# Optimization experiments

Hardware: AMD Instinct MI355X
Metric: run time of the kernel (lower is better)

Reference implementation:

```python
import jax, jax.numpy as jnp
import numpy as np

B, E, N, H, F = 16, 8192, 384, 32, 16


def _forward(edge_feat, node_feat, edge_index, edge_mask, num_ligand_atoms,
             structural_w, plip_protein_w, plip_ligand_w, plip_inter_w,
             loc_w, virtual_w, W1, b1, W2, b2):
    n_graph, max_e, _ = edge_feat.shape
    n_node = node_feat.shape[1]
    codes = edge_feat[:, :, :3].astype(jnp.int32)          # [B,E,3] edge type codes
    dist = edge_feat[:, :, 3:4]                            # [B,E,1]
    c0, c1, c2 = codes[..., 0], codes[..., 1], codes[..., 2]
    src = edge_index[:, 0, :]                              # [B,E]
    tgt = edge_index[:, 1, :]
    nl = num_ligand_atoms[:, None]
    src_lig = src < nl
    tgt_lig = tgt < nl

    # structural edges: c0 in {0,1} -> idx = c0*4 + c1*2 + c2
    struct_idx = jnp.clip(c0 * 4 + c1 * 2 + c2, 0, 19)
    struct_emb = structural_w[struct_idx]                  # [B,E,H]

    # PLIP edges: c0 == 5 -> table chosen by ligand membership + location emb
    pi = jnp.clip(c1, 0, 14)
    both_lig = src_lig & tgt_lig
    both_prot = (~src_lig) & (~tgt_lig)
    plip_emb = jnp.where(both_lig[..., None], plip_ligand_w[pi],
                         jnp.where(both_prot[..., None], plip_protein_w[pi], plip_inter_w[pi]))
    loc = jnp.where(both_lig, 0, jnp.where(both_prot, 1, 2))
    plip_emb = plip_emb + loc_w[loc]

    is_struct = (c0 == 0) | (c0 == 1)
    is_plip = c0 == 5
    type_emb = jnp.where(is_struct[..., None], struct_emb,
                         jnp.where(is_plip[..., None], plip_emb, 0.0))

    # distance MLP: Linear(1,H) -> ReLU -> Linear(H,H)
    h = jax.nn.relu(dist @ W1.T + b1)                      # [B,E,H]
    dist_emb = h @ W2.T + b2

    keep = edge_mask & ~((src == 0) & (tgt == 0))
    edge_emb = jnp.where(keep[..., None], type_emb + dist_emb, 0.0)  # [B,E,H]

    # scatter-add into bias [B, N+1, N+1, H] (symmetric), offset +1 for graph token
    s1 = src + 1
    t1 = tgt + 1
    valid = edge_mask & (src >= 0) & (src < n_node) & (tgt >= 0) & (tgt < n_node)
    s_idx = jnp.where(valid, s1, 0)
    t_idx = jnp.where(valid, t1, 0)
    val = jnp.where(valid[..., None], edge_emb, 0.0)
    b_idx = jnp.broadcast_to(jnp.arange(n_graph)[:, None], (n_graph, max_e))

    bias = jnp.zeros((n_graph, n_node + 1, n_node + 1, H), dtype=edge_feat.dtype)
    bias = bias.at[b_idx, s_idx, t_idx].add(val)
    bias = bias.at[b_idx, t_idx, s_idx].add(val)

    # graph-token virtual distance
    t = virtual_w[0]                                       # [H]
    bias = bias.at[:, 1:, 0, :].add(t)
    bias = bias.at[:, 0, :, :].add(t)
    return jnp.transpose(bias, (0, 3, 1, 2))               # [B,H,N+1,N+1]


def setup_inputs() -> dict:
    key = jax.random.key(0)
    ks = jax.random.split(key, 16)
    c0 = jax.random.randint(ks[0], (B, E), 0, 7)
    c1 = jnp.where(c0 <= 1, jax.random.randint(ks[1], (B, E), 0, 2),
                   jax.random.randint(ks[2], (B, E), 0, 15))
    c2 = jax.random.randint(ks[3], (B, E), 0, 2)
    dist = jax.random.uniform(ks[4], (B, E, 1)) * 10.0
    edge_feat = jnp.concatenate([jnp.stack([c0, c1, c2], -1).astype(jnp.float32), dist], -1)
    edge_index = jax.random.randint(ks[5], (B, 2, E), 0, N).astype(jnp.int32)
    edge_mask = jax.random.uniform(ks[6], (B, E)) > 0.1
    num_ligand_atoms = jax.random.randint(ks[7], (B,), 1, N).astype(jnp.int32)
    node_feat = jax.random.normal(ks[8], (B, N, F), dtype=jnp.float32)
    std_e = 0.02
    std_l = 0.02 / np.sqrt(12.0)
    structural_w = (jax.random.normal(ks[9], (20, H)) * std_e).at[0].set(0.0)
    plip_protein_w = (jax.random.normal(ks[10], (15, H)) * std_e).at[0].set(0.0)
    plip_ligand_w = (jax.random.normal(ks[11], (15, H)) * std_e).at[0].set(0.0)
    plip_inter_w = (jax.random.normal(ks[12], (15, H)) * std_e).at[0].set(0.0)
    loc_w = jax.random.normal(ks[13], (4, H)) * std_e
    virtual_w = jax.random.normal(ks[14], (1, H)) * std_e
    W1 = jax.random.normal(ks[15], (H, 1)) * std_l
    W2 = jax.random.normal(jax.random.fold_in(key, 99), (H, H)) * std_l
    b1 = jnp.zeros((H,), jnp.float32)
    b2 = jnp.zeros((H,), jnp.float32)
    return dict(edge_feat=edge_feat, node_feat=node_feat, edge_index=edge_index,
                edge_mask=edge_mask, num_ligand_atoms=num_ligand_atoms,
                structural_w=structural_w, plip_protein_w=plip_protein_w,
                plip_ligand_w=plip_ligand_w, plip_inter_w=plip_inter_w,
                loc_w=loc_w, virtual_w=virtual_w, W1=W1, b1=b1, W2=W2, b2=b2)


def reference(edge_feat, node_feat, edge_index, edge_mask, num_ligand_atoms,
              structural_w, plip_protein_w, plip_ligand_w, plip_inter_w,
              loc_w, virtual_w, W1, b1, W2, b2):
    return _forward(edge_feat, node_feat, edge_index, edge_mask, num_ligand_atoms,
                    structural_w, plip_protein_w, plip_ligand_w, plip_inter_w,
                    loc_w, virtual_w, W1, b1, W2, b2)
```

## Files before the change

### kernel.cpp

```cpp
#include <hip/hip_runtime.h>
#include <hip/hip_bf16.h>

#define B_  16
#define E_  8192
#define NN_ 384
#define N1_ 385
#define H_  32
#define HH_ 16
#define PLANE_ (N1_ * N1_)
#define TOTAL_ (B_ * H_ * PLANE_)
#define CAP_ 128
#define NBIN_ (B_ * N1_)
#define STRIDE_ 396
#define TS_ 21
#define CHUNK_ 5
#define NCH_ 77

#define WS_COUNTS 0
#define WS_T      32768
#define WS_A      33024
#define WS_B      (33024 + 33*32*4)
#define WS_BINS2  65536
#define WS_NEED   ((size_t)WS_BINS2 + (size_t)NBIN_*CAP_*8)


__global__ __launch_bounds__(256) void prep_kernel(
    const float* __restrict__ W1, const float* __restrict__ b1,
    const float* __restrict__ W2, const float* __restrict__ b2,
    float* __restrict__ T, float* __restrict__ A, float* __restrict__ Bv,
    int* __restrict__ counts)
{
    int g = blockIdx.x * 256 + threadIdx.x;
    if (g < NBIN_) counts[g] = 0;

    if (blockIdx.x == 0) {
        __shared__ float sTv[32], sT[32], sW1[32], sb1[32];
        int tid = threadIdx.x;
        if (tid < 32) {
            float w = W1[tid], b = b1[tid];
            sW1[tid] = w; sb1[tid] = b;
            sTv[tid] = (w != 0.0f) ? (-b / w) : -3.402823e38f;
        }
        __syncthreads();
        if (tid < 32) {
            float t = sTv[tid];
            int rank = 0;
            for (int j = 0; j < 32; ++j) {
                float tj = sTv[j];
                rank += (tj < t || (tj == t && j < tid)) ? 1 : 0;
            }
            sT[rank] = t;
        }
        __syncthreads();
        if (tid < 32) T[tid] = sT[tid];
        for (int idx = tid; idx < 33 * 32; idx += 256) {
            int s = idx >> 5, h = idx & 31;
            float m;
            if (s == 0)       m = sT[0] - 1.0f;
            else if (s == 32) m = sT[31] + 1.0f;
            else              m = 0.5f * (sT[s - 1] + sT[s]);
            float alpha = b2[h], beta = 0.0f;
            for (int k = 0; k < 32; ++k) {
                float w = sW1[k], b = sb1[k];
                bool act = (w > 0.0f) ? (m > -b / w)
                         : (w < 0.0f) ? (m < -b / w) : (b > 0.0f);
                if (act) {
                    float w2 = W2[h * 32 + k];
                    alpha = fmaf(w2, b, alpha);
                    beta  = fmaf(w2, w, beta);
                }
            }
            A[idx] = alpha; Bv[idx] = beta;
        }
    }
}

__global__ __launch_bounds__(256) void bin_kernel(
    const float4* __restrict__ edge_feat,
    const int*    __restrict__ edge_index,
    const void*   __restrict__ edge_mask,
    const int*    __restrict__ nlig,
    const float*  __restrict__ T,
    int* __restrict__ counts, int2* __restrict__ bins2)
{
    int lane = threadIdx.x & 63;
    int probe = ((const int*)edge_mask)[lane];
    bool byte_mask = __any(probe != 0 && probe != 1);

    int gid = blockIdx.x * blockDim.x + threadIdx.x;
    int b = gid >> 13, e = gid & (E_ - 1);
    bool m = byte_mask ? (((const unsigned char*)edge_mask)[gid] != 0)
                       : (((const int*)edge_mask)[gid] != 0);
    if (!m) return;
    int src = edge_index[(b * 2 + 0) * E_ + e];
    int tgt = edge_index[(b * 2 + 1) * E_ + e];
    if (src < 0 || src >= NN_ || tgt < 0 || tgt >= NN_) return;
    if (src == 0 && tgt == 0) return;

    float4 ef = edge_feat[gid];
    int c0 = (int)ef.x, c1 = (int)ef.y, c2 = (int)ef.z;
    float dist = ef.w;

    int r;
    if (c0 == 0 || c0 == 1) {
        r = min(max(c0 * 4 + c1 * 2 + c2, 0), 19);
    } else if (c0 == 5) {
        int pi = min(max(c1, 0), 14);
        int nl = nlig[b];
        bool sl = src < nl, tl = tgt < nl;
        int loc = (sl && tl) ? 0 : ((!sl && !tl) ? 1 : 2);
        r = 20 + loc * 15 + pi;
    } else r = 65;

    int lo = 0;
#pragma unroll
    for (int q = 0; q < 8; ++q) {
        float4 tv = *reinterpret_cast<const float4*>(T + 4 * q);
        lo += (tv.x < dist) ? 1 : 0;
        lo += (tv.y < dist) ? 1 : 0;
        lo += (tv.z < dist) ? 1 : 0;
        lo += (tv.w < dist) ? 1 : 0;
    }

    int s1 = src + 1, t1 = tgt + 1;
    int db = __float_as_int(dist);
    int base = (lo << 16) | (r << 9);
    int bin1 = b * N1_ + s1, bin2i = b * N1_ + t1;
    int p = atomicAdd(&counts[bin1], 1);
    if (p < CAP_) bins2[bin1 * CAP_ + p] = make_int2(base | t1, db);
    p = atomicAdd(&counts[bin2i], 1);
    if (p < CAP_) bins2[bin2i * CAP_ + p] = make_int2(base | s1, db);
}

__global__ __launch_bounds__(512, 8) void chunk_kernel(
    const float* __restrict__ structural_w,
    const float* __restrict__ plip_protein_w,
    const float* __restrict__ plip_ligand_w,
    const float* __restrict__ plip_inter_w,
    const float* __restrict__ loc_w,
    const float* __restrict__ virtual_w,
    const float* __restrict__ A,
    const float* __restrict__ Bv,
    const int*   __restrict__ counts,
    const int2*  __restrict__ bins2,
    float* __restrict__ out)
{
    __shared__ float4 srow4[HH_ * (STRIDE_ / 4)];
    __shared__ float sA[33 * TS_], sB[33 * TS_];
    __shared__ float sType[66 * TS_];
    float* srow = reinterpret_cast<float*>(srow4);

    int bid = blockIdx.x;
    int chunk = bid % NCH_;
    int rest  = bid / NCH_;
    int half = rest & 1;
    int b = rest >> 1;
    int h0 = half << 4;
    int tid = threadIdx.x;
    int wv = tid >> 6, lane = tid & 63;

    int i0 = chunk * CHUNK_;
    int rowid0 = b * N1_ + i0;

    int cnts[CHUNK_];
#pragma unroll
    for (int ii = 0; ii < CHUNK_; ++ii) cnts[ii] = counts[rowid0 + ii];

    for (int idx = tid; idx < 33 * 16; idx += 512) {
        int s = idx >> 4, hh = idx & 15;
        sA[s * TS_ + hh] = A[s * 32 + h0 + hh];
        sB[s * TS_ + hh] = Bv[s * 32 + h0 + hh];
    }
    for (int idx = tid; idx < 66 * 16; idx += 512) {
        int r = idx >> 4, hh = idx & 15;
        float v;
        if (r < 20) v = structural_w[r * 32 + h0 + hh];
        else if (r < 65) {
            int t2 = r - 20;
            int loc = t2 / 15, pi = t2 - loc * 15;
            const float* pw = (loc == 0) ? plip_ligand_w
                            : (loc == 1) ? plip_protein_w : plip_inter_w;
            v = pw[pi * 32 + h0 + hh] + loc_w[loc * 32 + h0 + hh];
        } else v = 0.0f;
        sType[r * TS_ + hh] = v;
    }

    int hh_q = lane & 1;
    int slot = lane >> 1;
    int hhg  = (wv << 1) | hh_q;
    int hq   = h0 + hhg;
    float* sW = srow + (wv << 1) * STRIDE_;

    int rw = lane >> 5;
    int sl = lane & 31;
    int hw = h0 + (wv << 1) + rw;
    float vw0 = virtual_w[h0 + (wv << 1)];
    float vw1 = virtual_w[h0 + (wv << 1) + 1];

    __syncthreads();

#pragma unroll 1
    for (int ii = 0; ii < CHUNK_; ++ii) {
        int i = i0 + ii;
        int rowid = rowid0 + ii;

#pragma unroll
        for (int r = 0; r < 2; ++r) {
            float vwr = (r == 0) ? vw0 : vw1;
            float fill = (i == 0) ? vwr : 0.0f;
            float4 f4 = make_float4(fill, fill, fill, fill);
            float4* rp = reinterpret_cast<float4*>(sW + r * STRIDE_);
            for (int c = lane; c < STRIDE_ / 4; c += 64) rp[c] = f4;
        }
        if (i != 0 && lane < 2) {
            int hr = h0 + (wv << 1) + lane;
            int off = (4 - ((hr + i) & 3)) & 3;
            sW[lane * STRIDE_ + 4 - off] = (lane == 0) ? vw0 : vw1;
        }

        int cnt = cnts[ii]; cnt = cnt < CAP_ ? cnt : CAP_;
        int offq = (4 - ((hq + i) & 3)) & 3;
        int base = hh_q * STRIDE_ + 4 - offq;
        for (int j = slot; j < cnt; j += 32) {
            int2 e2 = bins2[rowid * CAP_ + j];
            float dist = __int_as_float(e2.y);
            int other = e2.x & 0x1FF;
            int r     = (e2.x >> 9) & 0x7F;
            int lo    = e2.x >> 16;
            float acc = fmaf(dist, sB[lo * TS_ + hhg], sA[lo * TS_ + hhg])
                      + sType[r * TS_ + hhg];
            atomicAdd(&sW[base + other], acc);
        }

        {
            const float* rr = sW + rw * STRIDE_;
            float* dst = out + ((size_t)(b * H_ + hw)) * PLANE_ + (size_t)i * N1_;
            int off = (4 - ((hw + i) & 3)) & 3;
            if (sl < off) dst[sl] = rr[4 - off + sl];
            int nvec = (N1_ - off) >> 2;
            for (int q = sl; q < nvec; q += 32) {
                float4 v = *reinterpret_cast<const float4*>(rr + 4 + 4 * q);
                *reinterpret_cast<float4*>(dst + off + 4 * q) = v;
            }
            int done = off + (nvec << 2);
            int rem = N1_ - done;
            if (sl < rem) dst[done + sl] = rr[4 + 4 * nvec + sl];
        }
    }
}


__global__ __launch_bounds__(256) void init_out_kernel(
    float* __restrict__ out, const float* __restrict__ virtual_w)
{
    unsigned int tid = blockIdx.x * blockDim.x + threadIdx.x;
    unsigned int base = tid * 4u;
    if (base >= (unsigned int)TOTAL_) return;
    float4 v; float* pv = &v.x;
#pragma unroll
    for (int u = 0; u < 4; ++u) {
        unsigned int idx = base + u;
        unsigned int bh     = idx / (unsigned int)PLANE_;
        unsigned int within = idx - bh * (unsigned int)PLANE_;
        unsigned int h = bh & (H_ - 1);
        unsigned int i = within / (unsigned int)N1_;
        unsigned int j = within - i * (unsigned int)N1_;
        pv[u] = (i == 0u || j == 0u) ? virtual_w[h] : 0.0f;
    }
    *reinterpret_cast<float4*>(out + base) = v;
}

__global__ __launch_bounds__(256) void edge_kernel(
    const float4* __restrict__ edge_feat, const int* __restrict__ edge_index,
    const void* __restrict__ edge_mask, const int* __restrict__ nlig,
    const float* __restrict__ structural_w, const float* __restrict__ plip_protein_w,
    const float* __restrict__ plip_ligand_w, const float* __restrict__ plip_inter_w,
    const float* __restrict__ loc_w, const float* __restrict__ W1,
    const float* __restrict__ b1, const float* __restrict__ W2,
    const float* __restrict__ b2, float* __restrict__ out)
{
    __shared__ float sW2[H_ * H_];
    __shared__ float sW1[H_], sb1[H_], sb2[H_];
    __shared__ float sStruct[20 * H_];
    __shared__ float sPlipP[15 * H_], sPlipL[15 * H_], sPlipI[15 * H_];
    __shared__ float sLoc[4 * H_];

    for (int i = threadIdx.x; i < H_ * H_; i += blockDim.x) sW2[i] = W2[i];
    if (threadIdx.x < H_) {
        sW1[threadIdx.x] = W1[threadIdx.x];
        sb1[threadIdx.x] = b1[threadIdx.x];
        sb2[threadIdx.x] = b2[threadIdx.x];
    }
    for (int i = threadIdx.x; i < 20 * H_; i += blockDim.x) sStruct[i] = structural_w[i];
    for (int i = threadIdx.x; i < 15 * H_; i += blockDim.x) {
        sPlipP[i] = plip_protein_w[i]; sPlipL[i] = plip_ligand_w[i]; sPlipI[i] = plip_inter_w[i];
    }
    for (int i = threadIdx.x; i < 4 * H_; i += blockDim.x) sLoc[i] = loc_w[i];

    int lane = threadIdx.x & 63;
    int probe = ((const int*)edge_mask)[lane];
    bool byte_mask = __any(probe != 0 && probe != 1);
    __syncthreads();

    int gid = blockIdx.x * blockDim.x + threadIdx.x;
    int b = gid >> 13, e = gid & (E_ - 1);
    bool m = byte_mask ? (((const unsigned char*)edge_mask)[gid] != 0)
                       : (((const int*)edge_mask)[gid] != 0);
    if (!m) return;
    int src = edge_index[(b * 2 + 0) * E_ + e];
    int tgt = edge_index[(b * 2 + 1) * E_ + e];
    if (src < 0 || src >= NN_ || tgt < 0 || tgt >= NN_) return;
    if (src == 0 && tgt == 0) return;

    float4 ef = edge_feat[gid];
    int c0 = (int)ef.x, c1 = (int)ef.y, c2 = (int)ef.z;
    float dist = ef.w;
    const float* type_ptr = nullptr; const float* loc_ptr = nullptr;
    if (c0 == 0 || c0 == 1) {
        int si = min(max(c0 * 4 + c1 * 2 + c2, 0), 19);
        type_ptr = &sStruct[si * H_];
    } else if (c0 == 5) {
        int pi = min(max(c1, 0), 14);
        int nl = nlig[b];
        bool sl = src < nl, tl = tgt < nl;
        const float* pw; int loc;
        if (sl && tl)        { pw = sPlipL; loc = 0; }
        else if (!sl && !tl) { pw = sPlipP; loc = 1; }
        else                 { pw = sPlipI; loc = 2; }
        type_ptr = &pw[pi * H_]; loc_ptr = &sLoc[loc * H_];
    }
    float hk[H_];
#pragma unroll
    for (int k = 0; k < H_; ++k) {
        float v = fmaf(dist, sW1[k], sb1[k]);
        hk[k] = v > 0.0f ? v : 0.0f;
    }
    int s1 = src + 1, t1 = tgt + 1;
    float* outb = out + (size_t)b * H_ * PLANE_;
    int off1 = s1 * N1_ + t1, off2 = t1 * N1_ + s1;
#pragma unroll 4
    for (int h = 0; h < H_; ++h) {
        float acc = sb2[h];
#pragma unroll
        for (int k = 0; k < H_; ++k) acc = fmaf(hk[k], sW2[h * H_ + k], acc);
        if (type_ptr) acc += type_ptr[h];
        if (loc_ptr)  acc += loc_ptr[h];
        float* p = outb + (size_t)h * PLANE_;
        unsafeAtomicAdd(p + off1, acc);
        unsafeAtomicAdd(p + off2, acc);
    }
}

extern "C" void kernel_launch(void* const* d_in, const int* in_sizes, int n_in,
                              void* d_out, int out_size, void* d_ws, size_t ws_size,
                              hipStream_t stream)
{
    const float4* edge_feat      = (const float4*)d_in[0];
    const int*    edge_index     = (const int*)  d_in[2];
    const void*   edge_mask      =               d_in[3];
    const int*    nlig           = (const int*)  d_in[4];
    const float*  structural_w   = (const float*)d_in[5];
    const float*  plip_protein_w = (const float*)d_in[6];
    const float*  plip_ligand_w  = (const float*)d_in[7];
    const float*  plip_inter_w   = (const float*)d_in[8];
    const float*  loc_w          = (const float*)d_in[9];
    const float*  virtual_w      = (const float*)d_in[10];
    const float*  W1             = (const float*)d_in[11];
    const float*  b1             = (const float*)d_in[12];
    const float*  W2             = (const float*)d_in[13];
    const float*  b2             = (const float*)d_in[14];
    float* out = (float*)d_out;

    if (ws_size >= WS_NEED) {
        char* ws = (char*)d_ws;
        int*   counts = (int*)  (ws + WS_COUNTS);
        float* T      = (float*)(ws + WS_T);
        float* A      = (float*)(ws + WS_A);
        float* Bv     = (float*)(ws + WS_B);
        int2*  bins2  = (int2*) (ws + WS_BINS2);

        prep_kernel<<<25, 256, 0, stream>>>(W1, b1, W2, b2, T, A, Bv, counts);
        bin_kernel<<<(B_ * E_) / 256, 256, 0, stream>>>(
            edge_feat, edge_index, edge_mask, nlig, T, counts, bins2);
        chunk_kernel<<<B_ * 2 * NCH_, 512, 0, stream>>>(
            structural_w, plip_protein_w, plip_ligand_w, plip_inter_w,
            loc_w, virtual_w, A, Bv, counts, bins2, out);
    } else {
        unsigned int nth  = (unsigned int)(TOTAL_ / 4);
        unsigned int nblk = (nth + 255u) / 256u;
        init_out_kernel<<<nblk, 256, 0, stream>>>(out, virtual_w);
        edge_kernel<<<(B_ * E_) / 256, 256, 0, stream>>>(
            edge_feat, edge_index, edge_mask, nlig,
            structural_w, plip_protein_w, plip_ligand_w, plip_inter_w,
            loc_w, W1, b1, W2, b2, out);
    }
}
```

Before: 96.14 us.

## Use persistent grid-stride row loop with prefetched bins and nontemporal stores

Replaces the fixed chunked grid of blocks with a persistent 1024-block grid that strides over all rows. It prefetches the next row's count and first 64 bin entries into registers while the current row is processed, which hides global load latency. Output rows are written with nontemporal stores to avoid cache pollution. The trade-off is fewer, longer-lived blocks, with the shared tables loaded once per block and possible load imbalance across blocks.

```diff
diff --git a/kernel.cpp b/kernel.cpp
--- a/kernel.cpp
+++ b/kernel.cpp
@@ -13,8 +13,10 @@
 #define NBIN_ (B_ * N1_)
 #define STRIDE_ 396
 #define TS_ 21
-#define CHUNK_ 5
-#define NCH_ 77
+#define GBLK_ 1024
+#define RSTRIDE_ (GBLK_ / 2)
+
+typedef float vfloat4 __attribute__((ext_vector_type(4)));
 
 #define WS_COUNTS 0
 #define WS_T      32768
@@ -151,20 +153,11 @@
     float* srow = reinterpret_cast<float*>(srow4);
 
     int bid = blockIdx.x;
-    int chunk = bid % NCH_;
-    int rest  = bid / NCH_;
-    int half = rest & 1;
-    int b = rest >> 1;
+    int half = bid & 1;
+    int rbase = bid >> 1;
     int h0 = half << 4;
     int tid = threadIdx.x;
     int wv = tid >> 6, lane = tid & 63;
-
-    int i0 = chunk * CHUNK_;
-    int rowid0 = b * N1_ + i0;
-
-    int cnts[CHUNK_];
-#pragma unroll
-    for (int ii = 0; ii < CHUNK_; ++ii) cnts[ii] = counts[rowid0 + ii];
 
     for (int idx = tid; idx < 33 * 16; idx += 512) {
         int s = idx >> 4, hh = idx & 15;
@@ -197,12 +190,22 @@
     float vw0 = virtual_w[h0 + (wv << 1)];
     float vw1 = virtual_w[h0 + (wv << 1) + 1];
 
+    int rowid = rbase;
+    int cnt = counts[rowid];
+    int2 eA = bins2[rowid * CAP_ + slot];
+    int2 eB = bins2[rowid * CAP_ + slot + 32];
+
     __syncthreads();
 
-#pragma unroll 1
-    for (int ii = 0; ii < CHUNK_; ++ii) {
-        int i = i0 + ii;
-        int rowid = rowid0 + ii;
+    while (rowid < NBIN_) {
+        int rowid_n = rowid + RSTRIDE_;
+        int rn = rowid_n < NBIN_ ? rowid_n : 0;
+        int cnt_n = counts[rn];
+        int2 eA_n = bins2[rn * CAP_ + slot];
+        int2 eB_n = bins2[rn * CAP_ + slot + 32];
+
+        int b = rowid / N1_;
+        int i = rowid - b * N1_;
 
 #pragma unroll
         for (int r = 0; r < 2; ++r) {
@@ -218,10 +221,28 @@
             sW[lane * STRIDE_ + 4 - off] = (lane == 0) ? vw0 : vw1;
         }
 
-        int cnt = cnts[ii]; cnt = cnt < CAP_ ? cnt : CAP_;
+        int c = cnt < CAP_ ? cnt : CAP_;
         int offq = (4 - ((hq + i) & 3)) & 3;
         int base = hh_q * STRIDE_ + 4 - offq;
-        for (int j = slot; j < cnt; j += 32) {
+        if (slot < c) {
+            float dist = __int_as_float(eA.y);
+            int other = eA.x & 0x1FF;
+            int r     = (eA.x >> 9) & 0x7F;
+            int lo    = eA.x >> 16;
+            float acc = fmaf(dist, sB[lo * TS_ + hhg], sA[lo * TS_ + hhg])
+                      + sType[r * TS_ + hhg];
+            atomicAdd(&sW[base + other], acc);
+        }
+        if (slot + 32 < c) {
+            float dist = __int_as_float(eB.y);
+            int other = eB.x & 0x1FF;
+            int r     = (eB.x >> 9) & 0x7F;
+            int lo    = eB.x >> 16;
+            float acc = fmaf(dist, sB[lo * TS_ + hhg], sA[lo * TS_ + hhg])
+                      + sType[r * TS_ + hhg];
+            atomicAdd(&sW[base + other], acc);
+        }
+        for (int j = slot + 64; j < c; j += 32) {
             int2 e2 = bins2[rowid * CAP_ + j];
             float dist = __int_as_float(e2.y);
             int other = e2.x & 0x1FF;
@@ -236,16 +257,20 @@
             const float* rr = sW + rw * STRIDE_;
             float* dst = out + ((size_t)(b * H_ + hw)) * PLANE_ + (size_t)i * N1_;
             int off = (4 - ((hw + i) & 3)) & 3;
-            if (sl < off) dst[sl] = rr[4 - off + sl];
+            if (sl < off) __builtin_nontemporal_store(rr[4 - off + sl], dst + sl);
             int nvec = (N1_ - off) >> 2;
             for (int q = sl; q < nvec; q += 32) {
-                float4 v = *reinterpret_cast<const float4*>(rr + 4 + 4 * q);
-                *reinterpret_cast<float4*>(dst + off + 4 * q) = v;
+                vfloat4 v = *reinterpret_cast<const vfloat4*>(rr + 4 + 4 * q);
+                __builtin_nontemporal_store(v,
+                    reinterpret_cast<vfloat4*>(dst + off + 4 * q));
             }
             int done = off + (nvec << 2);
             int rem = N1_ - done;
-            if (sl < rem) dst[done + sl] = rr[4 + 4 * nvec + sl];
-        }
+            if (sl < rem)
+                __builtin_nontemporal_store(rr[4 + 4 * nvec + sl], dst + done + sl);
+        }
+
+        rowid = rowid_n; cnt = cnt_n; eA = eA_n; eB = eB_n;
     }
 }
 
@@ -382,7 +407,7 @@
         prep_kernel<<<25, 256, 0, stream>>>(W1, b1, W2, b2, T, A, Bv, counts);
         bin_kernel<<<(B_ * E_) / 256, 256, 0, stream>>>(
             edge_feat, edge_index, edge_mask, nlig, T, counts, bins2);
-        chunk_kernel<<<B_ * 2 * NCH_, 512, 0, stream>>>(
+        chunk_kernel<<<GBLK_, 512, 0, stream>>>(
             structural_w, plip_protein_w, plip_ligand_w, plip_inter_w,
             loc_w, virtual_w, A, Bv, counts, bins2, out);
     } else {
```

Result: slower. 148.5 us (+54.4%).
